# Performance work log

Hardware: AMD Instinct MI355X
Metric: run time of the kernel (lower is better)

## Reference

```python
import jax, jax.numpy as jnp
import numpy as np

D_IN = 512
D = 1024      # new_embed_dim
H = 16        # num_heads
HD = D // H   # head_dim


def setup_inputs() -> dict:
    key = jax.random.key(0)
    ks = jax.random.split(key, 16)
    g = lambda k, shape, fan: jax.random.normal(k, shape, jnp.float32) / np.sqrt(fan)
    return {
        "x1": jax.random.normal(ks[0], (16, 1, D_IN), jnp.float32),
        "x2": jax.random.normal(ks[1], (16, 4096, D_IN), jnp.float32),
        "x3": jax.random.normal(ks[2], (16, 4096, D_IN), jnp.float32),
        # embedding1 (for x1) and embedding2 (used for BOTH x2 and x3, per source)
        "We1": g(ks[3], (D_IN, D), D_IN), "be1": jnp.zeros((D,), jnp.float32),
        "We2": g(ks[4], (D_IN, D), D_IN), "be2": jnp.zeros((D,), jnp.float32),
        "Wq": g(ks[5], (D, D), D), "bq": jnp.zeros((D,), jnp.float32),
        "Wk": g(ks[6], (D, D), D), "bk": jnp.zeros((D,), jnp.float32),
        "Wv": g(ks[7], (D, D), D), "bv": jnp.zeros((D,), jnp.float32),
        "Wo": g(ks[8], (D, D), D), "bo": jnp.zeros((D,), jnp.float32),
    }


def reference(x1, x2, x3, We1, be1, We2, be2, Wq, bq, Wk, bk, Wv, bv, Wo, bo):
    B = x1.shape[0]
    # embeddings (x3 intentionally uses embedding2's weights, matching source)
    x1e = x1 @ We1 + be1                      # [B,1,D]
    x2e = x2 @ We2 + be2                      # [B,S,D]
    x3e = x3 @ We2 + be2                      # [B,S,D]
    q = (x1e @ Wq + bq).reshape(B, -1, H, HD).transpose(0, 2, 1, 3)  # [B,H,1,HD]
    k = (x2e @ Wk + bk).reshape(B, -1, H, HD).transpose(0, 2, 1, 3)  # [B,H,S,HD]
    v = (x3e @ Wv + bv).reshape(B, -1, H, HD).transpose(0, 2, 1, 3)  # [B,H,S,HD]
    scale = jnp.asarray(np.sqrt(HD), q.dtype)
    attn = jax.nn.softmax(jnp.einsum("bhqd,bhkd->bhqk", q, k) / scale, axis=-1)
    # dropout is identity at inference (keras training=False default)
    av = jnp.einsum("bhqk,bhkd->bhqd", attn, v)          # [B,H,1,HD]
    av = av.transpose(0, 2, 1, 3).reshape(B, -1, D)      # [B,1,D]
    out = av @ Wo + bo                                   # [B,1,D]
    return jnp.squeeze(out, axis=1)                      # [B,D]
```

## Files before the change

### kernel.cpp

```cpp
#include <hip/hip_runtime.h>


#define DIN 512
#define DD  1024
#define NH  16
#define HD  64
#define BB  16
#define SS  4096
#define NCH 64

__device__ __forceinline__ int wave_id() {
    return __builtin_amdgcn_readfirstlane((int)(threadIdx.x >> 6));
}

__device__ __forceinline__ void tile_transpose(const float* __restrict__ in,
                                               float* __restrict__ out,
                                               int R, int C, int rblk, int cblk) {
    __shared__ float tl[32][33];
    const int tx = threadIdx.x & 31, ty = threadIdx.x >> 5;
    const int c0 = cblk * 32, r0 = rblk * 32;
#pragma unroll
    for (int k = 0; k < 4; ++k)
        tl[ty + k * 8][tx] = in[(size_t)(r0 + ty + k * 8) * C + c0 + tx];
    __syncthreads();
#pragma unroll
    for (int k = 0; k < 4; ++k)
        out[(size_t)(c0 + ty + k * 8) * R + r0 + tx] = tl[tx][ty + k * 8];
}

__global__ __launch_bounds__(256) void k_prep(const float* __restrict__ We2,
                                              const float* __restrict__ Wk,
                                              const float* __restrict__ be1,
                                              const float* __restrict__ bq,
                                              const float* __restrict__ bv,
                                              const float* __restrict__ bo,
                                              float* __restrict__ We2t,
                                              float* __restrict__ WkT,
                                              float* __restrict__ x1e,
                                              float* __restrict__ qb,
                                              float* __restrict__ av,
                                              float* __restrict__ out) {
    const int bx = blockIdx.x;
    if (bx < 512) {
        tile_transpose(We2, We2t, DIN, DD, bx >> 5, bx & 31);
    } else if (bx < 1536) {
        const int lb = bx - 512;
        tile_transpose(Wk, WkT, DD, DD, lb >> 5, lb & 31);
    } else {
        const int b = bx - 1536;
#pragma unroll
        for (int k = 0; k < 4; ++k) {
            const int c = k * 256 + threadIdx.x;
            x1e[(size_t)b * DD + c] = be1[c];
            qb[(size_t)b * DD + c]  = bq[c];
            av[(size_t)b * DD + c]  = bv[c];
            out[(size_t)b * DD + c] = bo[c];
        }
    }
}

template <int K, int N, int KS, bool HASB>
__global__ __launch_bounds__(256) void k_bmv2(const float* __restrict__ in,
                                              const float* __restrict__ W,
                                              const float* __restrict__ bias,
                                              float* __restrict__ out) {
    const int l = threadIdx.x & 63;
    const int c = blockIdx.x * 64 + l;
    const int wv = wave_id();
    constexpr int KCH = K / KS;
    constexpr int SUB = KCH / 4;
    const float* inb = in + (size_t)blockIdx.y * 16 * K;
    float acc[16];
#pragma unroll
    for (int r = 0; r < 16; ++r) acc[r] = 0.f;
    const int i0 = blockIdx.z * KCH + wv * SUB;
#pragma unroll 4
    for (int i = i0; i < i0 + SUB; ++i) {
        const float wval = W[(size_t)i * N + c];
#pragma unroll
        for (int r = 0; r < 16; ++r) acc[r] += inb[(size_t)r * K + i] * wval;
    }
    __shared__ float red[4][16][64];
#pragma unroll
    for (int r = 0; r < 16; ++r) red[wv][r][l] = acc[r];
    __syncthreads();
#pragma unroll
    for (int k = 0; k < 4; ++k) {
        const int r = wv + k * 4;
        float v = red[0][r][l] + red[1][r][l] + red[2][r][l] + red[3][r][l];
        float* dst = out + ((size_t)blockIdx.y * 16 + r) * N + c;
        if (KS == 1) {
            if (HASB) v += bias[c];
            *dst = v;
        } else {
            atomicAdd(dst, v);
        }
    }
}

__global__ __launch_bounds__(256) void k_u2(const float* __restrict__ q,
                                            const float* __restrict__ WkT,
                                            float* __restrict__ u) {
    const int h = blockIdx.y;
    const int l = threadIdx.x & 63;
    const int c = blockIdx.x * 64 + l;
    const int wv = wave_id();
    float acc[16];
#pragma unroll
    for (int bb = 0; bb < 16; ++bb) acc[bb] = 0.f;
#pragma unroll 4
    for (int dk = 0; dk < 16; ++dk) {
        const int d = wv * 16 + dk;
        const float wval = WkT[(size_t)(h * HD + d) * DD + c];
#pragma unroll
        for (int bb = 0; bb < 16; ++bb)
            acc[bb] += q[(size_t)bb * DD + h * HD + d] * wval;
    }
    __shared__ float red[4][16][64];
#pragma unroll
    for (int bb = 0; bb < 16; ++bb) red[wv][bb][l] = acc[bb];
    __syncthreads();
#pragma unroll
    for (int k = 0; k < 4; ++k) {
        const int bb = wv + k * 4;
        float v = red[0][bb][l] + red[1][bb][l] + red[2][bb][l] + red[3][bb][l];
        u[((size_t)bb * NH + h) * DD + c] = v;
    }
}

__global__ __launch_bounds__(256, 4) void k_attn(const float* __restrict__ x2,
                                                 const float* __restrict__ x3,
                                                 const float* __restrict__ w,
                                                 float* __restrict__ gp,
                                                 float* __restrict__ mls) {
    __shared__ __align__(16) float4 tile[64 * 33];
    float* etab = (float*)tile;

    const int b = blockIdx.y, ch = blockIdx.x;
    const int l = threadIdx.x & 63;
    const int wv = wave_id();
    const int h0 = wv * 4;
    const int s0 = ch * 64;
    const float4* wp = (const float4*)(w + ((size_t)b * NH + h0) * DIN);
    const float4* x2f = (const float4*)x2 + ((size_t)b * SS + s0) * (DIN / 4);

    float a0 = 0.f, a1 = 0.f, a2 = 0.f, a3 = 0.f;
    for (int kt = 0; kt < 4; ++kt) {
#pragma unroll
        for (int k = 0; k < 8; ++k) {
            const int idx = threadIdx.x + k * 256;
            const int row = idx >> 5, c4 = idx & 31;
            tile[row * 33 + c4] = x2f[(size_t)row * 128 + kt * 32 + c4];
        }
        __syncthreads();
#pragma unroll 8
        for (int c4 = 0; c4 < 32; ++c4) {
            const float4 x = tile[l * 33 + c4];
            const float4 q0 = wp[kt * 32 + c4];
            const float4 q1 = wp[128 + kt * 32 + c4];
            const float4 q2 = wp[256 + kt * 32 + c4];
            const float4 q3 = wp[384 + kt * 32 + c4];
            a0 += x.x * q0.x + x.y * q0.y + x.z * q0.z + x.w * q0.w;
            a1 += x.x * q1.x + x.y * q1.y + x.z * q1.z + x.w * q1.w;
            a2 += x.x * q2.x + x.y * q2.y + x.z * q2.z + x.w * q2.w;
            a3 += x.x * q3.x + x.y * q3.y + x.z * q3.z + x.w * q3.w;
        }
        __syncthreads();
    }

    const float sc0 = a0 * 0.125f, sc1 = a1 * 0.125f;
    const float sc2 = a2 * 0.125f, sc3 = a3 * 0.125f;
    float mh[4] = {sc0, sc1, sc2, sc3};
#pragma unroll
    for (int k = 0; k < 4; ++k) {
#pragma unroll
        for (int off = 1; off < 64; off <<= 1)
            mh[k] = fmaxf(mh[k], __shfl_xor(mh[k], off));
    }

    const float4 ev = make_float4(__expf(sc0 - mh[0]), __expf(sc1 - mh[1]),
                                  __expf(sc2 - mh[2]), __expf(sc3 - mh[3]));
    *(float4*)&etab[(wv * 64 + l) * 4] = ev;

    const float4* xr = (const float4*)(x3 + ((size_t)b * SS + s0) * DIN);
    float acc[4][8];
#pragma unroll
    for (int k = 0; k < 4; ++k)
#pragma unroll
        for (int jj = 0; jj < 8; ++jj) acc[k][jj] = 0.f;
    float ls[4] = {0.f, 0.f, 0.f, 0.f};

    float4 pa = xr[l], pb = xr[64 + l];
    float4 na = xr[128 + l], nb = xr[192 + l];
#pragma unroll 4
    for (int j = 0; j < 64; ++j) {
        const float4 xa = pa, xb = pb;
        pa = na; pb = nb;
        const int jn = (j + 2 < 64) ? (j + 2) : 63;
        na = xr[(size_t)jn * 128 + l];
        nb = xr[(size_t)jn * 128 + 64 + l];
        const float4 e4 = *(const float4*)&etab[(wv * 64 + j) * 4];
        const float ee[4] = {e4.x, e4.y, e4.z, e4.w};
        const float xv[8] = {xa.x, xa.y, xa.z, xa.w, xb.x, xb.y, xb.z, xb.w};
#pragma unroll
        for (int k = 0; k < 4; ++k) {
            ls[k] += ee[k];
#pragma unroll
            for (int jj = 0; jj < 8; ++jj) acc[k][jj] += ee[k] * xv[jj];
        }
    }

    float* gb = gp + ((size_t)(b * NCH + ch) * NH + h0) * DIN;
#pragma unroll
    for (int k = 0; k < 4; ++k) {
        *(float4*)(gb + (size_t)k * DIN + 4 * l) =
            make_float4(acc[k][0], acc[k][1], acc[k][2], acc[k][3]);
        *(float4*)(gb + (size_t)k * DIN + 256 + 4 * l) =
            make_float4(acc[k][4], acc[k][5], acc[k][6], acc[k][7]);
    }
    if (l == 0) {
#pragma unroll
        for (int k = 0; k < 4; ++k) {
            float* dst = mls + (((size_t)b * NCH + ch) * NH + h0 + k) * 2;
            dst[0] = mh[k];
            dst[1] = ls[k];
        }
    }
}

__global__ __launch_bounds__(256) void k_greduce2(const float* __restrict__ gp,
                                                  const float* __restrict__ mls,
                                                  float* __restrict__ g) {
    const int bx = blockIdx.x;
    const int pair = bx >> 1;
    const int b = pair >> 4, h = pair & 15;
    const int i = (bx & 1) * 256 + threadIdx.x;
    const float* mbase = mls + ((size_t)b * NCH * NH + h) * 2;
    float M = -1e30f;
#pragma unroll 8
    for (int ch = 0; ch < NCH; ++ch)
        M = fmaxf(M, mbase[(size_t)ch * NH * 2]);
    float L = 0.f;
#pragma unroll 8
    for (int ch = 0; ch < NCH; ++ch)
        L += __expf(mbase[(size_t)ch * NH * 2] - M) * mbase[(size_t)ch * NH * 2 + 1];
    const float invL = 1.f / L;
    const float* gpb = gp + ((size_t)(b * NCH) * NH + h) * DIN + i;
    float acc = 0.f;
#pragma unroll 8
    for (int ch = 0; ch < NCH; ++ch)
        acc += __expf(mbase[(size_t)ch * NH * 2] - M) * gpb[(size_t)ch * NH * DIN];
    g[(size_t)pair * DIN + i] = acc * invL;
}

__global__ __launch_bounds__(256) void k_av_at(const float* __restrict__ G2,
                                               const float* __restrict__ Wv,
                                               float* __restrict__ av) {
    const int h = blockIdx.x;
    const int l = threadIdx.x & 63;
    const int wv = wave_id();
    const int c0 = blockIdx.y * 128 + wv * 32;
    float acc[16];
#pragma unroll
    for (int bb = 0; bb < 16; ++bb) acc[bb] = 0.f;
#pragma unroll 4
    for (int c = c0; c < c0 + 32; ++c) {
        const float wval = Wv[(size_t)c * DD + h * HD + l];
#pragma unroll
        for (int bb = 0; bb < 16; ++bb)
            acc[bb] += G2[((size_t)bb * NH + h) * DD + c] * wval;
    }
    __shared__ float red[4][16][64];
#pragma unroll
    for (int bb = 0; bb < 16; ++bb) red[wv][bb][l] = acc[bb];
    __syncthreads();
#pragma unroll
    for (int k = 0; k < 4; ++k) {
        const int bb = wv + k * 4;
        float v = red[0][bb][l] + red[1][bb][l] + red[2][bb][l] + red[3][bb][l];
        atomicAdd(&av[(size_t)bb * DD + h * HD + l], v);
    }
}

extern "C" void kernel_launch(void* const* d_in, const int* in_sizes, int n_in,
                              void* d_out, int out_size, void* d_ws, size_t ws_size,
                              hipStream_t stream) {
    const float* x1  = (const float*)d_in[0];
    const float* x2  = (const float*)d_in[1];
    const float* x3  = (const float*)d_in[2];
    const float* We1 = (const float*)d_in[3];
    const float* be1 = (const float*)d_in[4];
    const float* We2 = (const float*)d_in[5];
    const float* be2 = (const float*)d_in[6];
    const float* Wq  = (const float*)d_in[7];
    const float* bq  = (const float*)d_in[8];
    const float* Wk  = (const float*)d_in[9];
    const float* bk  = (const float*)d_in[10];
    const float* Wv  = (const float*)d_in[11];
    const float* bv  = (const float*)d_in[12];
    const float* Wo  = (const float*)d_in[13];
    const float* bo  = (const float*)d_in[14];
    (void)bk;
    float* out = (float*)d_out;

    char* ws = (char*)d_ws;
    size_t off = 0;
    auto alloc = [&](size_t bytes) -> void* {
        void* p = ws + off;
        off = (off + bytes + 255) & ~(size_t)255;
        return p;
    };
    float* We2t = (float*)alloc((size_t)DD * DIN * 4);
    float* WkT  = (float*)alloc((size_t)DD * DD * 4);
    float* x1e  = (float*)alloc((size_t)BB * DD * 4);
    float* qb   = (float*)alloc((size_t)BB * DD * 4);
    float* u    = (float*)alloc((size_t)BB * NH * DD * 4);
    float* wv_  = (float*)alloc((size_t)BB * NH * DIN * 4);
    float* g    = (float*)alloc((size_t)BB * NH * DIN * 4);
    float* G2   = (float*)alloc((size_t)BB * NH * DD * 4);
    float* av   = (float*)alloc((size_t)BB * DD * 4);
    float* gp   = (float*)alloc((size_t)BB * NCH * NH * DIN * 4);
    float* mls  = (float*)alloc((size_t)BB * NCH * NH * 2 * 4);

    k_prep<<<1552, 256, 0, stream>>>(We2, Wk, be1, bq, bv, bo,
                                     We2t, WkT, x1e, qb, av, out);
    k_bmv2<DIN, DD, 8, false><<<dim3(DD / 64, 1, 8), 256, 0, stream>>>(x1, We1, nullptr, x1e);
    k_bmv2<DD, DD, 8, false><<<dim3(DD / 64, 1, 8), 256, 0, stream>>>(x1e, Wq, nullptr, qb);
    k_u2<<<dim3(DD / 64, NH), 256, 0, stream>>>(qb, WkT, u);
    k_bmv2<DD, DIN, 1, false><<<dim3(DIN / 64, BB * NH / 16, 1), 256, 0, stream>>>(u, We2t, nullptr, wv_);
    k_attn<<<dim3(NCH, BB), 256, 0, stream>>>(x2, x3, wv_, gp, mls);
    k_greduce2<<<BB * NH * 2, 256, 0, stream>>>(gp, mls, g);
    k_bmv2<DIN, DD, 1, true><<<dim3(DD / 64, BB * NH / 16, 1), 256, 0, stream>>>(g, We2, be2, G2);
    k_av_at<<<dim3(NH, 8), 256, 0, stream>>>(G2, Wv, av);
    k_bmv2<DD, DD, 8, false><<<dim3(DD / 64, 1, 8), 256, 0, stream>>>(av, Wo, nullptr, out);
}
```

Before: 452.8 us.

## Double k_attn block to 512 threads and repartition value pass by column

```diff
diff --git a/kernel.cpp b/kernel.cpp
--- a/kernel.cpp
+++ b/kernel.cpp
@@ -128,27 +128,27 @@
     }
 }
 
-__global__ __launch_bounds__(256, 4) void k_attn(const float* __restrict__ x2,
+__global__ __launch_bounds__(512, 8) void k_attn(const float* __restrict__ x2,
                                                  const float* __restrict__ x3,
                                                  const float* __restrict__ w,
                                                  float* __restrict__ gp,
                                                  float* __restrict__ mls) {
     __shared__ __align__(16) float4 tile[64 * 33];
-    float* etab = (float*)tile;
+    __shared__ __align__(16) float etab[64 * 20];
 
     const int b = blockIdx.y, ch = blockIdx.x;
     const int l = threadIdx.x & 63;
     const int wv = wave_id();
-    const int h0 = wv * 4;
+    const int h0 = wv * 2;
     const int s0 = ch * 64;
     const float4* wp = (const float4*)(w + ((size_t)b * NH + h0) * DIN);
     const float4* x2f = (const float4*)x2 + ((size_t)b * SS + s0) * (DIN / 4);
 
-    float a0 = 0.f, a1 = 0.f, a2 = 0.f, a3 = 0.f;
+    float a0 = 0.f, a1 = 0.f;
     for (int kt = 0; kt < 4; ++kt) {
 #pragma unroll
-        for (int k = 0; k < 8; ++k) {
-            const int idx = threadIdx.x + k * 256;
+        for (int k = 0; k < 4; ++k) {
+            const int idx = threadIdx.x + k * 512;
             const int row = idx >> 5, c4 = idx & 31;
             tile[row * 33 + c4] = x2f[(size_t)row * 128 + kt * 32 + c4];
         }
@@ -158,74 +158,69 @@
             const float4 x = tile[l * 33 + c4];
             const float4 q0 = wp[kt * 32 + c4];
             const float4 q1 = wp[128 + kt * 32 + c4];
-            const float4 q2 = wp[256 + kt * 32 + c4];
-            const float4 q3 = wp[384 + kt * 32 + c4];
             a0 += x.x * q0.x + x.y * q0.y + x.z * q0.z + x.w * q0.w;
             a1 += x.x * q1.x + x.y * q1.y + x.z * q1.z + x.w * q1.w;
-            a2 += x.x * q2.x + x.y * q2.y + x.z * q2.z + x.w * q2.w;
-            a3 += x.x * q3.x + x.y * q3.y + x.z * q3.z + x.w * q3.w;
         }
         __syncthreads();
     }
 
     const float sc0 = a0 * 0.125f, sc1 = a1 * 0.125f;
-    const float sc2 = a2 * 0.125f, sc3 = a3 * 0.125f;
-    float mh[4] = {sc0, sc1, sc2, sc3};
-#pragma unroll
-    for (int k = 0; k < 4; ++k) {
-#pragma unroll
-        for (int off = 1; off < 64; off <<= 1)
-            mh[k] = fmaxf(mh[k], __shfl_xor(mh[k], off));
-    }
-
-    const float4 ev = make_float4(__expf(sc0 - mh[0]), __expf(sc1 - mh[1]),
-                                  __expf(sc2 - mh[2]), __expf(sc3 - mh[3]));
-    *(float4*)&etab[(wv * 64 + l) * 4] = ev;
-
-    const float4* xr = (const float4*)(x3 + ((size_t)b * SS + s0) * DIN);
-    float acc[4][8];
-#pragma unroll
-    for (int k = 0; k < 4; ++k)
-#pragma unroll
-        for (int jj = 0; jj < 8; ++jj) acc[k][jj] = 0.f;
-    float ls[4] = {0.f, 0.f, 0.f, 0.f};
-
-    float4 pa = xr[l], pb = xr[64 + l];
-    float4 na = xr[128 + l], nb = xr[192 + l];
+    float m0 = sc0, m1 = sc1;
+#pragma unroll
+    for (int off = 1; off < 64; off <<= 1) {
+        m0 = fmaxf(m0, __shfl_xor(m0, off));
+        m1 = fmaxf(m1, __shfl_xor(m1, off));
+    }
+    const float e0 = __expf(sc0 - m0), e1 = __expf(sc1 - m1);
+    etab[l * 20 + h0]     = e0;
+    etab[l * 20 + h0 + 1] = e1;
+    float ls0 = e0, ls1 = e1;
+#pragma unroll
+    for (int off = 1; off < 64; off <<= 1) {
+        ls0 += __shfl_xor(ls0, off);
+        ls1 += __shfl_xor(ls1, off);
+    }
+    if (l == 0) {
+        float* dst = mls + (((size_t)b * NCH + ch) * NH + h0) * 2;
+        dst[0] = m0; dst[1] = ls0;
+        dst[2] = m1; dst[3] = ls1;
+    }
+    __syncthreads();
+
+    const int col = wv * 64 + l;
+    const float* x3c = x3 + ((size_t)b * SS + s0) * DIN + col;
+    float acc[16];
+#pragma unroll
+    for (int h = 0; h < 16; ++h) acc[h] = 0.f;
+
+    float x0 = x3c[0];
+    float x1 = x3c[DIN];
+    float x2r = x3c[2 * DIN];
+    float x3r = x3c[3 * DIN];
 #pragma unroll 4
     for (int j = 0; j < 64; ++j) {
-        const float4 xa = pa, xb = pb;
-        pa = na; pb = nb;
-        const int jn = (j + 2 < 64) ? (j + 2) : 63;
-        na = xr[(size_t)jn * 128 + l];
-        nb = xr[(size_t)jn * 128 + 64 + l];
-        const float4 e4 = *(const float4*)&etab[(wv * 64 + j) * 4];
-        const float ee[4] = {e4.x, e4.y, e4.z, e4.w};
-        const float xv[8] = {xa.x, xa.y, xa.z, xa.w, xb.x, xb.y, xb.z, xb.w};
-#pragma unroll
-        for (int k = 0; k < 4; ++k) {
-            ls[k] += ee[k];
-#pragma unroll
-            for (int jj = 0; jj < 8; ++jj) acc[k][jj] += ee[k] * xv[jj];
-        }
-    }
-
-    float* gb = gp + ((size_t)(b * NCH + ch) * NH + h0) * DIN;
-#pragma unroll
-    for (int k = 0; k < 4; ++k) {
-        *(float4*)(gb + (size_t)k * DIN + 4 * l) =
-            make_float4(acc[k][0], acc[k][1], acc[k][2], acc[k][3]);
-        *(float4*)(gb + (size_t)k * DIN + 256 + 4 * l) =
-            make_float4(acc[k][4], acc[k][5], acc[k][6], acc[k][7]);
-    }
-    if (l == 0) {
-#pragma unroll
-        for (int k = 0; k < 4; ++k) {
-            float* dst = mls + (((size_t)b * NCH + ch) * NH + h0 + k) * 2;
-            dst[0] = mh[k];
-            dst[1] = ls[k];
-        }
-    }
+        const float xv = x0;
+        x0 = x1; x1 = x2r; x2r = x3r;
+        const int jn = (j + 4 < 64) ? (j + 4) : 63;
+        x3r = x3c[(size_t)jn * DIN];
+        const float4 ea = *(const float4*)&etab[j * 20];
+        const float4 eb = *(const float4*)&etab[j * 20 + 4];
+        const float4 ec = *(const float4*)&etab[j * 20 + 8];
+        const float4 ed = *(const float4*)&etab[j * 20 + 12];
+        acc[0]  += ea.x * xv;  acc[1]  += ea.y * xv;
+        acc[2]  += ea.z * xv;  acc[3]  += ea.w * xv;
+        acc[4]  += eb.x * xv;  acc[5]  += eb.y * xv;
+        acc[6]  += eb.z * xv;  acc[7]  += eb.w * xv;
+        acc[8]  += ec.x * xv;  acc[9]  += ec.y * xv;
+        acc[10] += ec.z * xv;  acc[11] += ec.w * xv;
+        acc[12] += ed.x * xv;  acc[13] += ed.y * xv;
+        acc[14] += ed.z * xv;  acc[15] += ed.w * xv;
+    }
+
+    float* gb = gp + ((size_t)(b * NCH + ch) * NH) * DIN + col;
+#pragma unroll
+    for (int h = 0; h < 16; ++h)
+        gb[(size_t)h * DIN] = acc[h];
 }
 
 __global__ __launch_bounds__(256) void k_greduce2(const float* __restrict__ gp,
@@ -328,7 +323,7 @@
     k_bmv2<DD, DD, 8, false><<<dim3(DD / 64, 1, 8), 256, 0, stream>>>(x1e, Wq, nullptr, qb);
     k_u2<<<dim3(DD / 64, NH), 256, 0, stream>>>(qb, WkT, u);
     k_bmv2<DD, DIN, 1, false><<<dim3(DIN / 64, BB * NH / 16, 1), 256, 0, stream>>>(u, We2t, nullptr, wv_);
-    k_attn<<<dim3(NCH, BB), 256, 0, stream>>>(x2, x3, wv_, gp, mls);
+    k_attn<<<dim3(NCH, BB), 512, 0, stream>>>(x2, x3, wv_, gp, mls);
     k_greduce2<<<BB * NH * 2, 256, 0, stream>>>(gp, mls, g);
     k_bmv2<DIN, DD, 1, true><<<dim3(DD / 64, BB * NH / 16, 1), 256, 0, stream>>>(g, We2, be2, G2);
     k_av_at<<<dim3(NH, 8), 256, 0, stream>>>(G2, Wv, av);
```

New measurement: 446.9 us. No clear change (-1.3%).
